# Performance work log

Measured on AMD Instinct MI355X. Metric: run time of the kernel, lower is better.

Reference implementation:

```python
import jax, jax.numpy as jnp
import numpy as np

N_NODES = 100000
N_EDGES = 500000
HID = 128


def setup_inputs() -> dict:
    key = jax.random.key(0)
    k = jax.random.split(key, 8)
    h = jax.random.normal(k[0], (N_NODES, HID), dtype=jnp.float32)
    src = jax.random.randint(k[1], (N_EDGES,), 0, N_NODES)
    dst = jax.random.randint(k[2], (N_EDGES,), 0, N_NODES)
    # torch nn.Linear weights are [out, in]
    W1 = jax.random.normal(k[3], (HID, 2 * HID), dtype=jnp.float32) * (1.0 / np.sqrt(2 * HID))
    b1 = jnp.zeros((HID,), dtype=jnp.float32)
    W2 = jax.random.normal(k[4], (1, HID), dtype=jnp.float32) * (1.0 / np.sqrt(HID))
    b2 = jnp.zeros((1,), dtype=jnp.float32)
    W3 = jax.random.normal(k[5], (1, 1), dtype=jnp.float32)
    b3 = jnp.zeros((1,), dtype=jnp.float32)
    return {"h": h, "src": src, "dst": dst, "W1": W1, "b1": b1, "W2": W2, "b2": b2, "W3": W3, "b3": b3}


def reference(h, src, dst, W1, b1, W2, b2, W3, b3):
    # gather src/dst node features per edge and concat -> [E, 2*HID]
    x = jnp.concatenate([h[src], h[dst]], axis=1)
    x = jax.nn.relu(x @ W1.T + b1)            # [E, HID]
    x = jax.nn.relu(x @ W2.T + b2)            # [E, 1]
    x = jax.nn.relu(x @ W3.T + b3)            # [E, 1]
    return jax.nn.sigmoid(x)                  # [E, 1]
```

## Files before the change

### kernel.cpp

```cpp
#include <hip/hip_runtime.h>
#include <hip/hip_bf16.h>


#define HID 128

using short8 = __attribute__((ext_vector_type(8))) short;
using f32x4  = __attribute__((ext_vector_type(4))) float;

typedef unsigned int uint32;

static __device__ __forceinline__ unsigned short f2bf(float f) {
    uint32 u = __float_as_uint(f);
    u += 0x7fffu + ((u >> 16) & 1u);
    return (unsigned short)(u >> 16);
}
static __device__ __forceinline__ uint32 pk2(float a, float b) {
    return ((uint32)f2bf(a)) | (((uint32)f2bf(b)) << 16);
}
static __device__ __forceinline__ float bflo(uint32 u) { return __uint_as_float(u << 16); }
static __device__ __forceinline__ float bfhi(uint32 u) { return __uint_as_float(u & 0xffff0000u); }

__global__ __launch_bounds__(256) void prep_kernel(
    const float* __restrict__ W1,
    const float* __restrict__ b1,
    unsigned short* __restrict__ wtab,
    float* __restrict__ bias256)
{
    const int idx  = blockIdx.x * 256 + threadIdx.x;
    const int widx = idx >> 6;
    const int lane = idx & 63;
    const int wave = widx >> 4;
    const int ot   = (widx >> 2) & 3;
    const int ks   = widx & 3;
    const int o    = wave * 64 + ot * 16 + (lane & 15);
    const int row  = o & 127;
    const int col  = ((o >= 128) ? 128 : 0) + ks * 32 + (lane >> 4) * 8;
    const float* p = W1 + row * 256 + col;
    float4 f0 = *(const float4*)p;
    float4 f1 = *(const float4*)(p + 4);
    uint4 st;
    st.x = pk2(f0.x, f0.y);
    st.y = pk2(f0.z, f0.w);
    st.z = pk2(f1.x, f1.y);
    st.w = pk2(f1.z, f1.w);
    *(uint4*)(wtab + (size_t)idx * 8) = st;

    if (idx < 256) bias256[idx] = (idx < 128) ? b1[idx] : 0.0f;
}

__global__ __launch_bounds__(256) void node_stage_v3_kernel(
    const float* __restrict__ h,
    const unsigned short* __restrict__ wtab,
    const float* __restrict__ bias256,
    unsigned short* __restrict__ AB,
    int N)
{
    __shared__ unsigned short hs[64 * 128];

    const int t    = threadIdx.x;
    const int lane = t & 63;
    const int wave = t >> 6;
    const int c    = lane & 15;
    const int q    = lane >> 4;

    short8 vfrag[4][4];
    float4 bias[4];
#pragma unroll
    for (int ot = 0; ot < 4; ++ot) {
#pragma unroll
        for (int ks = 0; ks < 4; ++ks) {
            int widx = (wave * 4 + ot) * 4 + ks;
            vfrag[ot][ks] = *(const short8*)(wtab + ((size_t)widx * 64 + lane) * 8);
        }
        bias[ot] = *(const float4*)(bias256 + wave * 64 + ot * 16 + q * 4);
    }

    const int n0 = blockIdx.x * 64;

    float4 g[8];
#pragma unroll
    for (int j = 0; j < 8; ++j) {
        int e4 = j * 256 + t;
        int rl = e4 >> 5;
        int grow = n0 + rl;
        if (grow >= N) grow = N - 1;
        g[j] = *(const float4*)(h + (size_t)grow * HID + (e4 & 31) * 4);
    }
#pragma unroll
    for (int j = 0; j < 8; ++j) {
        int e4 = j * 256 + t;
        int rl = e4 >> 5;
        int u  = e4 & 31;
        uint2 w2;
        w2.x = pk2(g[j].x, g[j].y);
        w2.y = pk2(g[j].z, g[j].w);
        *(uint2*)(hs + rl * 128 + ((u ^ ((rl & 15) << 1)) << 2)) = w2;
    }
    __syncthreads();

    f32x4 acc[4][4];
#pragma unroll
    for (int nt = 0; nt < 4; ++nt)
#pragma unroll
        for (int ot = 0; ot < 4; ++ot) acc[nt][ot] = (f32x4){0.f, 0.f, 0.f, 0.f};

#pragma unroll
    for (int ks = 0; ks < 4; ++ks) {
        short8 hfrag[4];
#pragma unroll
        for (int nt = 0; nt < 4; ++nt) {
            int r  = nt * 16 + c;
            int u0 = ks * 8 + q * 2;
            hfrag[nt] = *(const short8*)(hs + r * 128 + ((u0 ^ (c << 1)) << 2));
        }
#pragma unroll
        for (int nt = 0; nt < 4; ++nt)
#pragma unroll
            for (int ot = 0; ot < 4; ++ot)
                acc[nt][ot] = __builtin_amdgcn_mfma_f32_16x16x32_bf16(
                    vfrag[ot][ks], hfrag[nt], acc[nt][ot], 0, 0, 0);
    }

#pragma unroll
    for (int nt = 0; nt < 4; ++nt) {
        const int node = n0 + nt * 16 + c;
        if (node < N) {
#pragma unroll
            for (int ot = 0; ot < 4; ++ot) {
                int o_base = wave * 64 + ot * 16 + q * 4;
                uint2 st;
                st.x = pk2(acc[nt][ot][0] + bias[ot].x, acc[nt][ot][1] + bias[ot].y);
                st.y = pk2(acc[nt][ot][2] + bias[ot].z, acc[nt][ot][3] + bias[ot].w);
                *(uint2*)(AB + (size_t)node * 256 + o_base) = st;
            }
        }
    }
}

__global__ __launch_bounds__(256) void node_stage_kernel(
    const float* __restrict__ h,
    const float* __restrict__ W1,
    const float* __restrict__ b1,
    unsigned short* __restrict__ AB,
    int N)
{
    __shared__ unsigned short hsb[16 * 256];

    const int t    = threadIdx.x;
    const int lane = t & 63;
    const int wave = t >> 6;
    const int c    = lane & 15;
    const int q    = lane >> 4;

    short8 vfrag[4][4];
    float  bias[4][4];
#pragma unroll
    for (int ot = 0; ot < 4; ++ot) {
#pragma unroll
        for (int ks = 0; ks < 4; ++ks) {
            int o   = wave * 64 + ot * 16 + c;
            int row = o & 127;
            int col = ((o >= 128) ? 128 : 0) + ks * 32 + q * 8;
            const float* p = W1 + row * 256 + col;
            float4 f0 = *(const float4*)p;
            float4 f1 = *(const float4*)(p + 4);
            short8 v;
            v[0] = (short)f2bf(f0.x); v[1] = (short)f2bf(f0.y);
            v[2] = (short)f2bf(f0.z); v[3] = (short)f2bf(f0.w);
            v[4] = (short)f2bf(f1.x); v[5] = (short)f2bf(f1.y);
            v[6] = (short)f2bf(f1.z); v[7] = (short)f2bf(f1.w);
            vfrag[ot][ks] = v;
        }
#pragma unroll
        for (int r = 0; r < 4; ++r) {
            int o = wave * 64 + ot * 16 + q * 4 + r;
            bias[ot][r] = (o < 128) ? b1[o] : 0.0f;
        }
    }

    const int sr = t >> 4;
    const int sj = t & 15;
    const int ntiles = N >> 4;
    for (int tile = blockIdx.x; tile < ntiles; tile += gridDim.x) {
        int n0 = tile * 16;
        {
            const float* p = h + (size_t)(n0 + sr) * HID + sj * 8;
            float4 f0 = *(const float4*)p;
            float4 f1 = *(const float4*)(p + 4);
            uint4 st;
            st.x = pk2(f0.x, f0.y);
            st.y = pk2(f0.z, f0.w);
            st.z = pk2(f1.x, f1.y);
            st.w = pk2(f1.z, f1.w);
            *(uint4*)(hsb + sr * 256 + ((sj ^ sr) * 8)) = st;
        }
        __syncthreads();

        short8 hfrag[4];
#pragma unroll
        for (int ks = 0; ks < 4; ++ks) {
            int blk = (ks * 4 + q) ^ c;
            hfrag[ks] = *(const short8*)(hsb + c * 256 + blk * 8);
        }

        f32x4 acc[4];
#pragma unroll
        for (int ot = 0; ot < 4; ++ot) acc[ot] = (f32x4){0.f, 0.f, 0.f, 0.f};
#pragma unroll
        for (int ks = 0; ks < 4; ++ks)
#pragma unroll
            for (int ot = 0; ot < 4; ++ot)
                acc[ot] = __builtin_amdgcn_mfma_f32_16x16x32_bf16(
                    vfrag[ot][ks], hfrag[ks], acc[ot], 0, 0, 0);

        const int node = n0 + c;
#pragma unroll
        for (int ot = 0; ot < 4; ++ot) {
            int o_base = wave * 64 + ot * 16 + q * 4;
            uint2 st;
            st.x = pk2(acc[ot][0] + bias[ot][0], acc[ot][1] + bias[ot][1]);
            st.y = pk2(acc[ot][2] + bias[ot][2], acc[ot][3] + bias[ot][3]);
            *(uint2*)(AB + (size_t)node * 256 + o_base) = st;
        }
        __syncthreads();
    }
}

__global__ __launch_bounds__(256) void edge_stage_kernel(
    const unsigned short* __restrict__ AB,
    const int* __restrict__ src,
    const int* __restrict__ dst,
    const float* __restrict__ W2,
    const float* __restrict__ b2,
    const float* __restrict__ W3,
    const float* __restrict__ b3,
    float* __restrict__ out,
    int E)
{
    const int lane = threadIdx.x & 63;
    const int wave = threadIdx.x >> 6;
    const int sub  = lane & 7;
    const int eg   = lane >> 3;
    const int base = blockIdx.x * 64 + wave * 16;
    const int e0   = base + eg;
    const int e1   = base + 8 + eg;
    if (base >= E) return;
    const int ee0 = (e0 < E) ? e0 : (E - 1);
    const int ee1 = (e1 < E) ? e1 : (E - 1);

    const int s0 = src[ee0];
    const int d0 = dst[ee0];
    const int s1 = src[ee1];
    const int d1 = dst[ee1];

    const unsigned short* pa0 = AB + (size_t)s0 * 256 + sub * 16;
    const unsigned short* pb0 = AB + (size_t)d0 * 256 + 128 + sub * 16;
    const unsigned short* pa1 = AB + (size_t)s1 * 256 + sub * 16;
    const unsigned short* pb1 = AB + (size_t)d1 * 256 + 128 + sub * 16;

    const uint4 a00 = *(const uint4*)pa0;
    const uint4 a01 = *(const uint4*)(pa0 + 8);
    const uint4 b00 = *(const uint4*)pb0;
    const uint4 b01 = *(const uint4*)(pb0 + 8);
    const uint4 a10 = *(const uint4*)pa1;
    const uint4 a11 = *(const uint4*)(pa1 + 8);
    const uint4 b10 = *(const uint4*)pb1;
    const uint4 b11 = *(const uint4*)(pb1 + 8);

    const float4 w0  = *(const float4*)(W2 + sub * 16);
    const float4 w1  = *(const float4*)(W2 + sub * 16 + 4);
    const float4 w2v = *(const float4*)(W2 + sub * 16 + 8);
    const float4 w3v = *(const float4*)(W2 + sub * 16 + 12);

#define ACC8(p, ua, ub, wa, wb)                                   \
    {                                                             \
        float t0 = fmaxf(bflo(ua.x) + bflo(ub.x), 0.0f);          \
        float t1 = fmaxf(bfhi(ua.x) + bfhi(ub.x), 0.0f);          \
        float t2 = fmaxf(bflo(ua.y) + bflo(ub.y), 0.0f);          \
        float t3 = fmaxf(bfhi(ua.y) + bfhi(ub.y), 0.0f);          \
        float t4 = fmaxf(bflo(ua.z) + bflo(ub.z), 0.0f);          \
        float t5 = fmaxf(bfhi(ua.z) + bfhi(ub.z), 0.0f);          \
        float t6 = fmaxf(bflo(ua.w) + bflo(ub.w), 0.0f);          \
        float t7 = fmaxf(bfhi(ua.w) + bfhi(ub.w), 0.0f);          \
        p = fmaf(t0, wa.x, p);                                    \
        p = fmaf(t1, wa.y, p);                                    \
        p = fmaf(t2, wa.z, p);                                    \
        p = fmaf(t3, wa.w, p);                                    \
        p = fmaf(t4, wb.x, p);                                    \
        p = fmaf(t5, wb.y, p);                                    \
        p = fmaf(t6, wb.z, p);                                    \
        p = fmaf(t7, wb.w, p);                                    \
    }

    float p0 = 0.0f, p1 = 0.0f;
    ACC8(p0, a00, b00, w0, w1);
    ACC8(p0, a01, b01, w2v, w3v);
    ACC8(p1, a10, b10, w0, w1);
    ACC8(p1, a11, b11, w2v, w3v);
#undef ACC8

#pragma unroll
    for (int m = 4; m >= 1; m >>= 1) {
        p0 += __shfl_xor(p0, m, 64);
        p1 += __shfl_xor(p1, m, 64);
    }

    if (sub == 0) {
        const float bb2 = b2[0], ww3 = W3[0], bb3 = b3[0];
        if (e0 < E) {
            float y2 = fmaxf(p0 + bb2, 0.0f);
            float y3 = fmaxf(ww3 * y2 + bb3, 0.0f);
            out[e0] = 1.0f / (1.0f + __expf(-y3));
        }
        if (e1 < E) {
            float y2 = fmaxf(p1 + bb2, 0.0f);
            float y3 = fmaxf(ww3 * y2 + bb3, 0.0f);
            out[e1] = 1.0f / (1.0f + __expf(-y3));
        }
    }
}

__global__ __launch_bounds__(256) void edge_direct_kernel(
    const float* __restrict__ h,
    const int* __restrict__ src,
    const int* __restrict__ dst,
    const float* __restrict__ W1,
    const float* __restrict__ b1,
    const float* __restrict__ W2,
    const float* __restrict__ b2,
    const float* __restrict__ W3,
    const float* __restrict__ b3,
    float* __restrict__ out,
    int E)
{
    __shared__ float x[256];
    __shared__ float red[4];
    const int e = blockIdx.x;
    if (e >= E) return;
    const int t = threadIdx.x;
    const int s = src[e];
    const int d = dst[e];

    if (t < 128) x[t] = h[(size_t)s * HID + t];
    else         x[t] = h[(size_t)d * HID + (t - 128)];
    __syncthreads();

    float contrib = 0.0f;
    if (t < 128) {
        float acc = b1[t];
        const float* wr = W1 + t * 256;
        for (int k = 0; k < 256; ++k) acc = fmaf(wr[k], x[k], acc);
        contrib = fmaxf(acc, 0.0f) * W2[t];
    }
#pragma unroll
    for (int m = 32; m >= 1; m >>= 1) contrib += __shfl_xor(contrib, m, 64);
    if ((t & 63) == 0) red[t >> 6] = contrib;
    __syncthreads();
    if (t == 0) {
        float p = red[0] + red[1] + red[2] + red[3];
        float y2 = fmaxf(p + b2[0], 0.0f);
        float y3 = fmaxf(W3[0] * y2 + b3[0], 0.0f);
        out[e] = 1.0f / (1.0f + __expf(-y3));
    }
}

extern "C" void kernel_launch(void* const* d_in, const int* in_sizes, int n_in,
                              void* d_out, int out_size, void* d_ws, size_t ws_size,
                              hipStream_t stream) {
    const float* h   = (const float*)d_in[0];
    const int*   src = (const int*)d_in[1];
    const int*   dst = (const int*)d_in[2];
    const float* W1  = (const float*)d_in[3];
    const float* b1  = (const float*)d_in[4];
    const float* W2  = (const float*)d_in[5];
    const float* b2  = (const float*)d_in[6];
    const float* W3  = (const float*)d_in[7];
    const float* b3  = (const float*)d_in[8];
    float* out = (float*)d_out;

    const int N = in_sizes[0] / HID;
    const int E = in_sizes[1];

    const size_t ab_bytes   = (size_t)N * 256 * sizeof(unsigned short);
    const size_t wtab_off   = (ab_bytes + 255) & ~(size_t)255;
    const size_t wtab_bytes = (size_t)64 * 64 * 8 * sizeof(unsigned short);
    const size_t bias_off   = wtab_off + wtab_bytes;
    const size_t need_v2    = bias_off + 256 * sizeof(float);

    if (need_v2 <= ws_size) {
        unsigned short* AB   = (unsigned short*)d_ws;
        unsigned short* wtab = (unsigned short*)((char*)d_ws + wtab_off);
        float* bias256       = (float*)((char*)d_ws + bias_off);
        prep_kernel<<<16, 256, 0, stream>>>(W1, b1, wtab, bias256);
        const int nblocks = (N + 63) / 64;
        node_stage_v3_kernel<<<nblocks, 256, 0, stream>>>(h, wtab, bias256, AB, N);
        edge_stage_kernel<<<(E + 63) / 64, 256, 0, stream>>>(AB, src, dst, W2, b2, W3, b3, out, E);
    } else if (ab_bytes <= ws_size) {
        unsigned short* AB = (unsigned short*)d_ws;
        node_stage_kernel<<<1563, 256, 0, stream>>>(h, W1, b1, AB, N);
        edge_stage_kernel<<<(E + 63) / 64, 256, 0, stream>>>(AB, src, dst, W2, b2, W3, b3, out, E);
    } else {
        edge_direct_kernel<<<E, 256, 0, stream>>>(h, src, dst, W1, b1, W2, b2, W3, b3, out, E);
    }
}
```

Measured before the change: 152.9 us.

## Quantize per-node projected features to int8 with per-node scales

The node stage now stores its projected src/dst halves as int8 with a per-node, per-half absmax scale instead of bf16. A new edge kernel dequantizes the gathered rows before the ReLU and W2 dot product. This halves the bytes written by the node stage and gathered per edge, which is the dominant random-access traffic. In exchange it adds quantization error to the hidden activations, extra shared-memory staging and syncs for the absmax reduction, and a separate scale gather per edge.

Measured after the change: 129.7 us. 1.18x faster.

```diff
diff --git a/kernel.cpp b/kernel.cpp
--- a/kernel.cpp
+++ b/kernel.cpp
@@ -19,6 +19,9 @@
 }
 static __device__ __forceinline__ float bflo(uint32 u) { return __uint_as_float(u << 16); }
 static __device__ __forceinline__ float bfhi(uint32 u) { return __uint_as_float(u & 0xffff0000u); }
+static __device__ __forceinline__ float sb2f(uint32 u, int k) {
+    return (float)(signed char)((u >> (k * 8)) & 0xffu);
+}
 
 __global__ __launch_bounds__(256) void prep_kernel(
     const float* __restrict__ W1,
@@ -48,14 +51,17 @@
     if (idx < 256) bias256[idx] = (idx < 128) ? b1[idx] : 0.0f;
 }
 
-__global__ __launch_bounds__(256) void node_stage_v3_kernel(
+__global__ __launch_bounds__(256) void node_stage_i8_kernel(
     const float* __restrict__ h,
     const unsigned short* __restrict__ wtab,
     const float* __restrict__ bias256,
-    unsigned short* __restrict__ AB,
+    signed char* __restrict__ AB8,
+    float2* __restrict__ scales,
     int N)
 {
     __shared__ unsigned short hs[64 * 128];
+    __shared__ uint32 ab8u[64 * 64];
+    __shared__ float  wmax[4][4][16];
 
     const int t    = threadIdx.x;
     const int lane = t & 63;
@@ -121,18 +127,163 @@
                     vfrag[ot][ks], hfrag[nt], acc[nt][ot], 0, 0, 0);
     }
 
+    float lmax[4];
 #pragma unroll
     for (int nt = 0; nt < 4; ++nt) {
-        const int node = n0 + nt * 16 + c;
-        if (node < N) {
-#pragma unroll
-            for (int ot = 0; ot < 4; ++ot) {
-                int o_base = wave * 64 + ot * 16 + q * 4;
-                uint2 st;
-                st.x = pk2(acc[nt][ot][0] + bias[ot].x, acc[nt][ot][1] + bias[ot].y);
-                st.y = pk2(acc[nt][ot][2] + bias[ot].z, acc[nt][ot][3] + bias[ot].w);
-                *(uint2*)(AB + (size_t)node * 256 + o_base) = st;
-            }
+        float m = 0.0f;
+#pragma unroll
+        for (int ot = 0; ot < 4; ++ot) {
+            acc[nt][ot][0] += bias[ot].x;
+            acc[nt][ot][1] += bias[ot].y;
+            acc[nt][ot][2] += bias[ot].z;
+            acc[nt][ot][3] += bias[ot].w;
+            m = fmaxf(m, fabsf(acc[nt][ot][0]));
+            m = fmaxf(m, fabsf(acc[nt][ot][1]));
+            m = fmaxf(m, fabsf(acc[nt][ot][2]));
+            m = fmaxf(m, fabsf(acc[nt][ot][3]));
+        }
+        m = fmaxf(m, __shfl_xor(m, 16, 64));
+        m = fmaxf(m, __shfl_xor(m, 32, 64));
+        lmax[nt] = m;
+    }
+    if (q == 0) {
+#pragma unroll
+        for (int nt = 0; nt < 4; ++nt) wmax[wave][nt][c] = lmax[nt];
+    }
+    __syncthreads();
+
+    const int hw = (wave >> 1) * 2;
+    float inv[4];
+#pragma unroll
+    for (int nt = 0; nt < 4; ++nt) {
+        float m = fmaxf(wmax[hw][nt][c], wmax[hw + 1][nt][c]);
+        inv[nt] = (m > 0.0f) ? (127.0f / m) : 0.0f;
+    }
+
+    if (t < 64) {
+        int nt2 = t >> 4, c2 = t & 15;
+        if (n0 + t < N) {
+            float ma = fmaxf(wmax[0][nt2][c2], wmax[1][nt2][c2]);
+            float mb = fmaxf(wmax[2][nt2][c2], wmax[3][nt2][c2]);
+            scales[n0 + t] = make_float2(ma * (1.0f / 127.0f), mb * (1.0f / 127.0f));
+        }
+    }
+
+#pragma unroll
+    for (int nt = 0; nt < 4; ++nt) {
+        const int rowl = nt * 16 + c;
+#pragma unroll
+        for (int ot = 0; ot < 4; ++ot) {
+            int q0 = __float2int_rn(acc[nt][ot][0] * inv[nt]);
+            int q1 = __float2int_rn(acc[nt][ot][1] * inv[nt]);
+            int q2 = __float2int_rn(acc[nt][ot][2] * inv[nt]);
+            int q3 = __float2int_rn(acc[nt][ot][3] * inv[nt]);
+            uint32 packed = (uint32)(q0 & 255) | ((uint32)(q1 & 255) << 8) |
+                            ((uint32)(q2 & 255) << 16) | ((uint32)(q3 & 255) << 24);
+            int uidx = wave * 16 + ot * 4 + q;
+            ab8u[rowl * 64 + (uidx ^ ((rowl & 7) << 3))] = packed;
+        }
+    }
+    __syncthreads();
+
+#pragma unroll
+    for (int j = 0; j < 4; ++j) {
+        const int rowl = j * 16 + (t >> 4);
+        const int grow = n0 + rowl;
+        if (grow < N) {
+            const int u0 = 4 * (t & 15);
+            uint4 st;
+            st.x = ab8u[rowl * 64 + ((u0 + 0) ^ ((rowl & 7) << 3))];
+            st.y = ab8u[rowl * 64 + ((u0 + 1) ^ ((rowl & 7) << 3))];
+            st.z = ab8u[rowl * 64 + ((u0 + 2) ^ ((rowl & 7) << 3))];
+            st.w = ab8u[rowl * 64 + ((u0 + 3) ^ ((rowl & 7) << 3))];
+            *(uint4*)(AB8 + (size_t)grow * 256 + (t & 15) * 16) = st;
+        }
+    }
+}
+
+__global__ __launch_bounds__(256) void edge_stage_i8_kernel(
+    const signed char* __restrict__ AB8,
+    const float2* __restrict__ scales,
+    const int* __restrict__ src,
+    const int* __restrict__ dst,
+    const float* __restrict__ W2,
+    const float* __restrict__ b2,
+    const float* __restrict__ W3,
+    const float* __restrict__ b3,
+    float* __restrict__ out,
+    int E)
+{
+    const int lane = threadIdx.x & 63;
+    const int wave = threadIdx.x >> 6;
+    const int sub  = lane & 7;
+    const int eg   = lane >> 3;
+    const int base = blockIdx.x * 64 + wave * 16;
+    const int e0   = base + eg;
+    const int e1   = base + 8 + eg;
+    if (base >= E) return;
+    const int ee0 = (e0 < E) ? e0 : (E - 1);
+    const int ee1 = (e1 < E) ? e1 : (E - 1);
+
+    const int s0 = src[ee0];
+    const int d0 = dst[ee0];
+    const int s1 = src[ee1];
+    const int d1 = dst[ee1];
+
+    const uint4 a0 = *(const uint4*)(AB8 + (size_t)s0 * 256 + sub * 16);
+    const uint4 b0 = *(const uint4*)(AB8 + (size_t)d0 * 256 + 128 + sub * 16);
+    const uint4 a1 = *(const uint4*)(AB8 + (size_t)s1 * 256 + sub * 16);
+    const uint4 b1 = *(const uint4*)(AB8 + (size_t)d1 * 256 + 128 + sub * 16);
+    const float sa0 = scales[s0].x;
+    const float sb0 = scales[d0].y;
+    const float sa1 = scales[s1].x;
+    const float sb1 = scales[d1].y;
+
+    const float4 w0  = *(const float4*)(W2 + sub * 16);
+    const float4 w1  = *(const float4*)(W2 + sub * 16 + 4);
+    const float4 w2v = *(const float4*)(W2 + sub * 16 + 8);
+    const float4 w3v = *(const float4*)(W2 + sub * 16 + 12);
+
+#define ACCU4(p, ua, ub, wv, sa, sb)                                          \
+    {                                                                         \
+        float t0 = fmaxf(fmaf(sb2f(ua, 0), sa, sb2f(ub, 0) * sb), 0.0f);      \
+        float t1 = fmaxf(fmaf(sb2f(ua, 1), sa, sb2f(ub, 1) * sb), 0.0f);      \
+        float t2 = fmaxf(fmaf(sb2f(ua, 2), sa, sb2f(ub, 2) * sb), 0.0f);      \
+        float t3 = fmaxf(fmaf(sb2f(ua, 3), sa, sb2f(ub, 3) * sb), 0.0f);      \
+        p = fmaf(t0, wv.x, p);                                                \
+        p = fmaf(t1, wv.y, p);                                                \
+        p = fmaf(t2, wv.z, p);                                                \
+        p = fmaf(t3, wv.w, p);                                                \
+    }
+
+    float p0 = 0.0f, p1 = 0.0f;
+    ACCU4(p0, a0.x, b0.x, w0, sa0, sb0);
+    ACCU4(p0, a0.y, b0.y, w1, sa0, sb0);
+    ACCU4(p0, a0.z, b0.z, w2v, sa0, sb0);
+    ACCU4(p0, a0.w, b0.w, w3v, sa0, sb0);
+    ACCU4(p1, a1.x, b1.x, w0, sa1, sb1);
+    ACCU4(p1, a1.y, b1.y, w1, sa1, sb1);
+    ACCU4(p1, a1.z, b1.z, w2v, sa1, sb1);
+    ACCU4(p1, a1.w, b1.w, w3v, sa1, sb1);
+#undef ACCU4
+
+#pragma unroll
+    for (int m = 4; m >= 1; m >>= 1) {
+        p0 += __shfl_xor(p0, m, 64);
+        p1 += __shfl_xor(p1, m, 64);
+    }
+
+    if (sub == 0) {
+        const float bb2 = b2[0], ww3 = W3[0], bb3 = b3[0];
+        if (e0 < E) {
+            float y2 = fmaxf(p0 + bb2, 0.0f);
+            float y3 = fmaxf(ww3 * y2 + bb3, 0.0f);
+            out[e0] = 1.0f / (1.0f + __expf(-y3));
+        }
+        if (e1 < E) {
+            float y2 = fmaxf(p1 + bb2, 0.0f);
+            float y3 = fmaxf(ww3 * y2 + bb3, 0.0f);
+            out[e1] = 1.0f / (1.0f + __expf(-y3));
         }
     }
 }
@@ -381,21 +532,27 @@
     const int N = in_sizes[0] / HID;
     const int E = in_sizes[1];
 
-    const size_t ab_bytes   = (size_t)N * 256 * sizeof(unsigned short);
-    const size_t wtab_off   = (ab_bytes + 255) & ~(size_t)255;
-    const size_t wtab_bytes = (size_t)64 * 64 * 8 * sizeof(unsigned short);
-    const size_t bias_off   = wtab_off + wtab_bytes;
-    const size_t need_v2    = bias_off + 256 * sizeof(float);
-
-    if (need_v2 <= ws_size) {
-        unsigned short* AB   = (unsigned short*)d_ws;
-        unsigned short* wtab = (unsigned short*)((char*)d_ws + wtab_off);
-        float* bias256       = (float*)((char*)d_ws + bias_off);
+    const size_t ab8_bytes  = (size_t)N * 256;
+    const size_t sc_off     = (ab8_bytes + 255) & ~(size_t)255;
+    const size_t sc_bytes   = (size_t)N * sizeof(float2);
+    const size_t wt_off     = (sc_off + sc_bytes + 255) & ~(size_t)255;
+    const size_t wt_bytes   = (size_t)64 * 64 * 8 * sizeof(unsigned short);
+    const size_t bi_off     = wt_off + wt_bytes;
+    const size_t need_i8    = bi_off + 256 * sizeof(float);
+
+    const size_t ab16_bytes = (size_t)N * 256 * sizeof(unsigned short);
+
+    if (need_i8 <= ws_size) {
+        signed char*    AB8     = (signed char*)d_ws;
+        float2*         scales  = (float2*)((char*)d_ws + sc_off);
+        unsigned short* wtab    = (unsigned short*)((char*)d_ws + wt_off);
+        float*          bias256 = (float*)((char*)d_ws + bi_off);
         prep_kernel<<<16, 256, 0, stream>>>(W1, b1, wtab, bias256);
-        const int nblocks = (N + 63) / 64;
-        node_stage_v3_kernel<<<nblocks, 256, 0, stream>>>(h, wtab, bias256, AB, N);
-        edge_stage_kernel<<<(E + 63) / 64, 256, 0, stream>>>(AB, src, dst, W2, b2, W3, b3, out, E);
-    } else if (ab_bytes <= ws_size) {
+        node_stage_i8_kernel<<<(N + 63) / 64, 256, 0, stream>>>(
+            h, wtab, bias256, AB8, scales, N);
+        edge_stage_i8_kernel<<<(E + 63) / 64, 256, 0, stream>>>(
+            AB8, scales, src, dst, W2, b2, W3, b3, out, E);
+    } else if (ab16_bytes <= ws_size) {
         unsigned short* AB = (unsigned short*)d_ws;
         node_stage_kernel<<<1563, 256, 0, stream>>>(h, W1, b1, AB, N);
         edge_stage_kernel<<<(E + 63) / 64, 256, 0, stream>>>(AB, src, dst, W2, b2, W3, b3, out, E);
```
